# Kernel optimization log

Measured on AMD Instinct MI355X. Metric: run time of the kernel, lower is better.

Reference implementation:

```python
import jax, jax.numpy as jnp
import numpy as np

B = 1024      # graphs (frames)
P = 23        # nodes per frame (22 players + ball)
N = B * P     # total nodes
F = 14        # input node features
D = 256       # hidden dim
H = 4         # attention heads
Dh = D // H   # per-head dim
L = 3         # GATv2 layers
C = 23        # receiver classes
NEG_SLOPE = 0.2


def setup_inputs() -> dict:
    key = jax.random.key(0)
    ks = jax.random.split(key, 20)
    x = jax.random.normal(ks[0], (N, F), jnp.float32)
    # complete directed graph (no self loops) within each frame
    a = np.arange(P)
    s, d = np.meshgrid(a, a, indexing='ij')
    m = s != d
    s, d = s[m], d[m]                      # [P*(P-1)] = 506
    offs = (np.arange(B) * P)[:, None]
    src = (s[None, :] + offs).reshape(-1)
    dst = (d[None, :] + offs).reshape(-1)
    edge_index = jnp.asarray(np.stack([src, dst]), jnp.int32)   # [2, E]
    batch = jnp.asarray(np.repeat(np.arange(B), P), jnp.int32)  # [N]
    g = lambda k, shape, fan: jax.random.normal(k, shape, jnp.float32) / np.sqrt(fan)
    return {
        'x': x, 'edge_index': edge_index, 'batch': batch,
        # input projection F -> D
        'W_in': g(ks[1], (F, D), F), 'b_in': jnp.zeros((D,), jnp.float32),
        # stacked GATv2 layer params (all D -> D)
        'Wl': g(ks[2], (L, D, H, Dh), D), 'Wr': g(ks[3], (L, D, H, Dh), D),
        'att': g(ks[4], (L, H, Dh), Dh),
        # receiver head: D -> D -> C
        'Wr1': g(ks[5], (D, D), D), 'br1': jnp.zeros((D,), jnp.float32),
        'Wr2': g(ks[6], (D, C), D), 'br2': jnp.zeros((C,), jnp.float32),
        # shot head: receiver embedding + concat MLP 2D -> D -> 1
        'E_recv': g(ks[7], (C, D), D),
        'Ws1': g(ks[8], (2 * D, D), 2 * D), 'bs1': jnp.zeros((D,), jnp.float32),
        'Ws2': g(ks[9], (D, 1), D), 'bs2': jnp.zeros((1,), jnp.float32),
    }


def _gatv2_layer(h, src, dst, Wl, Wr, att):
    # GATv2: e_ij = a^T LeakyReLU(Wl h_j + Wr h_i); msg = alpha_ij * Wl h_j
    hl = jnp.einsum('nd,dhk->nhk', h, Wl)               # [N,H,Dh]
    hr = jnp.einsum('nd,dhk->nhk', h, Wr)
    e = jax.nn.leaky_relu(hl[src] + hr[dst], NEG_SLOPE) # [E,H,Dh]
    scores = jnp.einsum('ehk,hk->eh', e, att)           # [E,H]
    # segment softmax over incoming edges of each dst node
    smax = jax.ops.segment_max(scores, dst, num_segments=N)   # [N,H]
    ex = jnp.exp(scores - smax[dst])
    denom = jax.ops.segment_sum(ex, dst, num_segments=N)      # [N,H]
    alpha = ex / denom[dst]                                    # [E,H]
    msg = hl[src] * alpha[..., None]                           # [E,H,Dh]
    out = jax.ops.segment_sum(msg, dst, num_segments=N).reshape(N, H * Dh)
    return jax.nn.elu(out + h)  # residual + activation


def reference(x, edge_index, batch, W_in, b_in, Wl, Wr, att,
              Wr1, br1, Wr2, br2, E_recv, Ws1, bs1, Ws2, bs2):
    src, dst = edge_index[0], edge_index[1]
    h = x @ W_in + b_in                                   # [N,D]
    for l in range(L):
        h = _gatv2_layer(h, src, dst, Wl[l], Wr[l], att[l])
    # mean readout per graph
    cnt = jax.ops.segment_sum(jnp.ones((N,), h.dtype), batch, num_segments=B)
    g = jax.ops.segment_sum(h, batch, num_segments=B) / cnt[:, None]  # [B,D]
    # receiver distribution
    recv_logits = jax.nn.relu(g @ Wr1 + br1) @ Wr2 + br2  # [B,C]
    recv_probs = jax.nn.softmax(recv_logits, axis=1)
    # shot logit for every (graph, receiver) pair, fully batched
    z = jnp.concatenate([
        jnp.broadcast_to(g[:, None, :], (B, C, D)),
        jnp.broadcast_to(E_recv[None, :, :], (B, C, D)),
    ], axis=-1)                                           # [B,C,2D]
    shot_bc = (jax.nn.relu(z @ Ws1 + bs1) @ Ws2 + bs2)[..., 0]  # [B,C]
    # marginalize: expected shot logit under receiver distribution
    return jnp.sum(shot_bc * recv_probs, axis=1)          # [B]
```

## Files before the change

### kernel.cpp

```cpp
#include <hip/hip_runtime.h>

#define BBATCH 1024
#define NPAIR 512
#define PP 23
#define FF 14
#define DD 256
#define CC 23

#define HSTR 258
#define SLSTR 264
#define RG 47472
#define SL_OFF    (RG)
#define SRO_OFF   (RG + 12144)
#define FRAG_OFF  (RG)
#define ALPHA_OFF (RG + 24576)
#define XS_OFF    (ALPHA_OFF)
#define INVZ_OFF  (ALPHA_OFF + 8192)
#define SMEM_SZ   (INVZ_OFF + 384)

#define SWZB(b) ((b) ^ (((b) >> 3) & 7))
#define SWZC(c) (SWZB((c) >> 3) * 8 + ((c) & 7))

typedef _Float16 f16;
typedef __attribute__((ext_vector_type(8))) _Float16 f16x8;
typedef __attribute__((ext_vector_type(4))) _Float16 f16x4;
typedef __attribute__((ext_vector_type(2))) _Float16 f16x2;
typedef __attribute__((ext_vector_type(4))) float f32x4;

__global__ __launch_bounds__(256) void k_prep(const float* __restrict__ Wl,
    const float* __restrict__ Wr, const float* __restrict__ E,
    const float* __restrict__ Ws1, f16* __restrict__ Bf, float* __restrict__ EB)
{
    __shared__ float ws[DD][16];
    int t = threadIdx.x;
    if (blockIdx.x < 96) {
        int bid = blockIdx.x;
        int ll = bid >> 5, ntile = bid & 31;
        int n0 = ntile * 16;
        const float* W = (n0 < 256) ? (Wl + (size_t)ll * 65536) : (Wr + (size_t)ll * 65536);
        int c0 = n0 & 255;
        for (int kk = t >> 4; kk < DD; kk += 16)
            ws[kk][t & 15] = W[(size_t)kk * 256 + c0 + (t & 15)];
        __syncthreads();
        size_t base = (size_t)bid * 4096;
        for (int idx = t; idx < 4096; idx += 256) {
            int ks = idx >> 9;
            int lane = (idx >> 3) & 63;
            int e = idx & 7;
            int col = lane & 15;
            int k = ks * 32 + ((lane >> 4) << 3) + e;
            Bf[base + idx] = (f16)ws[k][col];
        }
    } else {
        int c = blockIdx.x - 96;
        float acc = 0.f;
        for (int k = 0; k < DD; ++k)
            acc = fmaf(E[c * DD + k], Ws1[(DD + k) * DD + t], acc);
        EB[c * DD + t] = acc;
    }
}

__global__ __launch_bounds__(512, 4) void k_fused(
    const float* __restrict__ x, const float* __restrict__ Win,
    const float* __restrict__ bin, const f16* __restrict__ Bf,
    const float* __restrict__ att, float* __restrict__ g)
{
    __shared__ __align__(16) char smem[SMEM_SZ];
    float* hstate = (float*)smem;
    f16* sl16   = (f16*)(smem + SL_OFF);
    f16* sro16  = (f16*)(smem + SRO_OFF);
    f16* frag   = (f16*)(smem + FRAG_OFF);
    f16* aF     = (f16*)(smem + ALPHA_OFF);
    float* xs   = (float*)(smem + XS_OFF);
    float* invZ = (float*)(smem + INVZ_OFF);

    int t = threadIdx.x;
    int pair = blockIdx.x;

    for (int idx = t; idx < 46 * FF; idx += 512)
        xs[idx] = x[(size_t)pair * 46 * FF + idx];
    __syncthreads();

    {
        int c2 = (t & 127) * 2, rp = t >> 7;
        float2 bb = *(const float2*)&bin[c2];
        for (int r = rp; r < 48; r += 4) {
            float h0 = 0.f, h1 = 0.f;
            if (r < 46) {
                h0 = bb.x; h1 = bb.y;
#pragma unroll
                for (int f = 0; f < FF; ++f) {
                    float xv = xs[r * FF + f];
                    float2 wv = *(const float2*)&Win[f * DD + c2];
                    h0 = fmaf(xv, wv.x, h0);
                    h1 = fmaf(xv, wv.y, h1);
                }
                *(float2*)&hstate[r * HSTR + c2] = make_float2(h0, h1);
            }
            int off = ((r >> 4) * 8 + (c2 >> 5)) * 512 +
                      ((r & 15) + (((c2 & 31) >> 3) << 4)) * 8 + (c2 & 7);
            f16x2 hv2 = { (f16)h0, (f16)h1 };
            *(f16x2*)(frag + off) = hv2;
        }
    }

    int ln = t & 63, w = t >> 6;

    int sc_i  = t >> 4;
    int sc_ch = t & 15;
    int sc_hh = sc_ch >> 2;
    bool sc_act = (t < 368);
    int sb0 = SWZB(2 * sc_ch) * 8;
    int sb1 = SWZB(2 * sc_ch + 1) * 8;

    for (int layer = 0; layer < 3; ++layer) {
        if (layer > 0) {
            int c2 = (t & 127) * 2, rp = t >> 7;
            for (int r = rp; r < 48; r += 4) {
                float h0 = 0.f, h1 = 0.f;
                if (r < 46) {
                    float2 hv = *(const float2*)&hstate[r * HSTR + c2];
                    h0 = hv.x; h1 = hv.y;
                }
                int off = ((r >> 4) * 8 + (c2 >> 5)) * 512 +
                          ((r & 15) + (((c2 & 31) >> 3) << 4)) * 8 + (c2 & 7);
                f16x2 hv2 = { (f16)h0, (f16)h1 };
                *(f16x2*)(frag + off) = hv2;
            }
        }
        __syncthreads();

        if (layer == 0)
            *(f32x4*)(smem + ALPHA_OFF + t * 16) = (f32x4)0.f;

        const f16* pB = Bf + (size_t)layer * 131072 + (size_t)(w * 4) * 4096 + ln * 8;
        const f16* lA = frag + ln * 8;

        f32x4 acc[3][4];
#pragma unroll
        for (int mt = 0; mt < 3; ++mt)
#pragma unroll
            for (int nt = 0; nt < 4; ++nt) acc[mt][nt] = (f32x4)0.0f;

        __builtin_amdgcn_s_setprio(1);
#pragma unroll
        for (int ks = 0; ks < 8; ++ks) {
            f16x8 a0 = *(const f16x8*)(lA + (0 * 8 + ks) * 512);
            f16x8 a1 = *(const f16x8*)(lA + (1 * 8 + ks) * 512);
            f16x8 a2 = *(const f16x8*)(lA + (2 * 8 + ks) * 512);
#pragma unroll
            for (int nt = 0; nt < 4; ++nt) {
                f16x8 b = *(const f16x8*)(pB + (nt * 8 + ks) * 512);
                acc[0][nt] = __builtin_amdgcn_mfma_f32_16x16x32_f16(a0, b, acc[0][nt], 0, 0, 0);
                acc[1][nt] = __builtin_amdgcn_mfma_f32_16x16x32_f16(a1, b, acc[1][nt], 0, 0, 0);
                acc[2][nt] = __builtin_amdgcn_mfma_f32_16x16x32_f16(a2, b, acc[2][nt], 0, 0, 0);
            }
        }
        __builtin_amdgcn_s_setprio(0);
        __syncthreads();

        for (int f = 0; f < 2; ++f) {
#pragma unroll
            for (int mt = 0; mt < 3; ++mt) {
                int rbase = mt * 16 + (ln >> 4) * 4;
#pragma unroll
                for (int nt = 0; nt < 4; ++nt) {
                    int col = w * 64 + nt * 16 + (ln & 15);
                    f16* dst = (col < 256) ? sl16 : sro16;
                    int cc = col & 255;
                    int sc = SWZC(cc);
#pragma unroll
                    for (int r2 = 0; r2 < 4; ++r2) {
                        int i = rbase + r2 - f * PP;
                        if (0 <= i && i < PP) dst[i * SLSTR + sc] = (f16)acc[mt][nt][r2];
                    }
                }
            }
            __syncthreads();

            if (sc_act) {
                const float* ap = att + layer * DD + sc_ch * 16;
                float4 af0 = *(const float4*)(ap);
                float4 af1 = *(const float4*)(ap + 4);
                float4 af2 = *(const float4*)(ap + 8);
                float4 af3 = *(const float4*)(ap + 12);
                f16x8 av0 = { (f16)af0.x, (f16)af0.y, (f16)af0.z, (f16)af0.w,
                              (f16)af1.x, (f16)af1.y, (f16)af1.z, (f16)af1.w };
                f16x8 av1 = { (f16)af2.x, (f16)af2.y, (f16)af2.z, (f16)af2.w,
                              (f16)af3.x, (f16)af3.y, (f16)af3.z, (f16)af3.w };
                const f16* srp = sro16 + sc_i * SLSTR;
                f16x8 rv0 = *(const f16x8*)(srp + sb0);
                f16x8 rv1 = *(const f16x8*)(srp + sb1);
                int wbase = ((sc_hh * 2 + (sc_i >> 4)) << 9) + ((sc_i & 15) << 3);
#pragma unroll 2
                for (int j = 0; j < PP; ++j) {
                    const f16* slp = sl16 + j * SLSTR;
                    f16x8 v0 = *(const f16x8*)(slp + sb0) + rv0;
                    f16x8 v1 = *(const f16x8*)(slp + sb1) + rv1;
                    v0 = __builtin_elementwise_max(v0, v0 * (f16)0.2f);
                    v1 = __builtin_elementwise_max(v1, v1 * (f16)0.2f);
                    f16x8 tot = av0 * v0;
                    tot += av1 * v1;
                    f16x4 t4 = __builtin_shufflevector(tot, tot, 0, 1, 2, 3) +
                               __builtin_shufflevector(tot, tot, 4, 5, 6, 7);
                    float p = (float)t4[0] + (float)t4[1] + (float)t4[2] + (float)t4[3];
                    p += __shfl_xor(p, 1, 64);
                    p += __shfl_xor(p, 2, 64);
                    if ((t & 3) == 0)
                        aF[wbase + ((j >> 3) << 7) + (j & 7)] =
                            (j == sc_i) ? (f16)(-60000.0f) : (f16)p;
                }
            }
            __syncthreads();

            if (t < 368) {
                int i = t >> 4, hh = (t >> 2) & 3, q = t & 3;
                int base = ((hh * 2 + (i >> 4)) << 9) + ((i & 15) << 3);
                float m = -1e30f;
                for (int j = q; j < PP; j += 4)
                    m = fmaxf(m, (float)aF[base + ((j >> 3) << 7) + (j & 7)]);
                m = fmaxf(m, __shfl_xor(m, 1, 64));
                m = fmaxf(m, __shfl_xor(m, 2, 64));
                float s = 0.f;
                for (int j = q; j < PP; j += 4) {
                    f16* p = aF + base + ((j >> 3) << 7) + (j & 7);
                    f16 e = (f16)__expf((float)*p - m);
                    *p = e;
                    s += (float)e;
                }
                s += __shfl_xor(s, 1, 64);
                s += __shfl_xor(s, 2, 64);
                if (q == 0) invZ[i * 4 + hh] = 1.f / s;
            }
            __syncthreads();

            {
                int h = w >> 1, mt = w & 1;
                f16x8 afrag = *(const f16x8*)(aF + ((h * 2 + mt) << 9) + ln * 8);
                int k0 = (ln >> 4) * 8;
                int cb = h * 64 + (ln & 15);
                __builtin_amdgcn_s_setprio(1);
#pragma unroll
                for (int nt = 0; nt < 4; ++nt) {
                    int c = cb + nt * 16;
                    int scn = SWZC(c);
                    f16x8 bfrag;
#pragma unroll
                    for (int e = 0; e < 8; ++e)
                        bfrag[e] = sl16[(k0 + e) * SLSTR + scn];
                    f32x4 a4 = __builtin_amdgcn_mfma_f32_16x16x32_f16(
                        afrag, bfrag, (f32x4)0.0f, 0, 0, 0);
#pragma unroll
                    for (int r2 = 0; r2 < 4; ++r2) {
                        int i = mt * 16 + (ln >> 4) * 4 + r2;
                        if (i < PP) {
                            int r = f * PP + i;
                            float res = a4[r2] * invZ[i * 4 + h] + hstate[r * HSTR + c];
                            hstate[r * HSTR + c] = (res > 0.f) ? res : (__expf(res) - 1.f);
                        }
                    }
                }
                __builtin_amdgcn_s_setprio(0);
            }
            __syncthreads();
        }
    }

    {
        int f = t >> 8, c = t & 255;
        float s = 0.f;
#pragma unroll
        for (int i = 0; i < PP; ++i) s += hstate[(f * PP + i) * HSTR + c];
        g[(size_t)(pair * 2 + f) * DD + c] = s * (1.0f / 23.0f);
    }
}

__global__ __launch_bounds__(256) void k_head(const float* __restrict__ g,
    const float* __restrict__ Wr1, const float* __restrict__ br1,
    const float* __restrict__ Wr2, const float* __restrict__ br2,
    const float* __restrict__ Ws1, const float* __restrict__ bs1,
    const float* __restrict__ Ws2, const float* __restrict__ bs2,
    const float* __restrict__ EB, float* __restrict__ out)
{
    __shared__ float gs[4][DD], t1s[4][DD], gtop[4][DD];
    __shared__ float logits[4][CC], probs[4][CC];
    __shared__ float red[4][4];
    int b0 = blockIdx.x * 4;
    int t = threadIdx.x;
    for (int idx = t; idx < 4 * DD; idx += 256)
        gs[idx >> 8][idx & 255] = g[(size_t)b0 * DD + idx];
    __syncthreads();

    float a1[4] = {0.f, 0.f, 0.f, 0.f}, a2[4] = {0.f, 0.f, 0.f, 0.f};
    for (int k = 0; k < DD; k += 2) {
        float w1a = Wr1[k * DD + t], w1b = Wr1[(k + 1) * DD + t];
        float w2a = Ws1[k * DD + t], w2b = Ws1[(k + 1) * DD + t];
#pragma unroll
        for (int gg = 0; gg < 4; ++gg) {
            float2 gv = *(const float2*)&gs[gg][k];
            a1[gg] = fmaf(gv.x, w1a, a1[gg]);
            a1[gg] = fmaf(gv.y, w1b, a1[gg]);
            a2[gg] = fmaf(gv.x, w2a, a2[gg]);
            a2[gg] = fmaf(gv.y, w2b, a2[gg]);
        }
    }
#pragma unroll
    for (int gg = 0; gg < 4; ++gg) {
        t1s[gg][t] = fmaxf(a1[gg] + br1[t], 0.f);
        gtop[gg][t] = a2[gg] + bs1[t];
    }
    __syncthreads();

    if (t < 4 * CC) {
        int gg = t / CC, c = t - gg * CC;
        float acc = br2[c];
        for (int d = 0; d < DD; ++d) acc = fmaf(t1s[gg][d], Wr2[d * CC + c], acc);
        logits[gg][c] = acc;
    }
    __syncthreads();
    if (t < 4 * CC) {
        int gg = t / CC, c = t - gg * CC;
        float m = -1e30f;
        for (int cc = 0; cc < CC; ++cc) m = fmaxf(m, logits[gg][cc]);
        float s = 0.f;
        for (int cc = 0; cc < CC; ++cc) s += __expf(logits[gg][cc] - m);
        probs[gg][c] = __expf(logits[gg][c] - m) / s;
    }
    __syncthreads();

    float wd = Ws2[t];
    float sacc[4];
#pragma unroll
    for (int gg = 0; gg < 4; ++gg) {
        float gt = gtop[gg][t];
        float acc = 0.f;
#pragma unroll
        for (int c = 0; c < CC; ++c)
            acc = fmaf(probs[gg][c], fmaxf(gt + EB[c * DD + t], 0.f), acc);
        sacc[gg] = acc * wd;
    }
#pragma unroll
    for (int gg = 0; gg < 4; ++gg) {
        float v = sacc[gg];
#pragma unroll
        for (int off = 32; off > 0; off >>= 1) v += __shfl_down(v, off, 64);
        if ((t & 63) == 0) red[t >> 6][gg] = v;
    }
    __syncthreads();
    if (t < 4)
        out[b0 + t] = red[0][t] + red[1][t] + red[2][t] + red[3][t] + bs2[0];
}

extern "C" void kernel_launch(void* const* d_in, const int* in_sizes, int n_in,
                              void* d_out, int out_size, void* d_ws, size_t ws_size,
                              hipStream_t stream)
{
    const float* x     = (const float*)d_in[0];
    const float* Win   = (const float*)d_in[3];
    const float* bin   = (const float*)d_in[4];
    const float* Wl    = (const float*)d_in[5];
    const float* Wr    = (const float*)d_in[6];
    const float* att   = (const float*)d_in[7];
    const float* Wr1   = (const float*)d_in[8];
    const float* br1   = (const float*)d_in[9];
    const float* Wr2   = (const float*)d_in[10];
    const float* br2   = (const float*)d_in[11];
    const float* Erecv = (const float*)d_in[12];
    const float* Ws1   = (const float*)d_in[13];
    const float* bs1   = (const float*)d_in[14];
    const float* Ws2   = (const float*)d_in[15];
    const float* bs2   = (const float*)d_in[16];
    float* out = (float*)d_out;

    f16* Bf   = (f16*)d_ws;
    float* g  = (float*)(Bf + (size_t)3 * 131072);
    float* EB = g + (size_t)BBATCH * DD;

    k_prep<<<dim3(96 + CC), dim3(256), 0, stream>>>(Wl, Wr, Erecv, Ws1, Bf, EB);
    k_fused<<<dim3(NPAIR), dim3(512), 0, stream>>>(x, Win, bin, Bf, att, g);
    k_head<<<dim3(256), dim3(256), 0, stream>>>(g, Wr1, br1, Wr2, br2,
                                                Ws1, bs1, Ws2, bs2, EB, out);
}
```

Before: 150.0 us.

## Fuse readout head MLPs into the main GATv2 kernel

Moves the receiver and shot head computation into the end of the fused GNN kernel, so each block computes its two graphs' outputs directly from the pooled embedding kept in shared memory. This removes the separate head kernel launch and the global round trip of the pooled features g. In exchange, each block now streams Wr1 and Ws1 itself for only two graphs instead of four, which raises total weight traffic through L2. It also reuses variables `ln` and `w`, which are presumably defined earlier in the kernel.

```diff
diff --git a/kernel.cpp b/kernel.cpp
--- a/kernel.cpp
+++ b/kernel.cpp
@@ -17,6 +17,13 @@
 #define XS_OFF    (ALPHA_OFF)
 #define INVZ_OFF  (ALPHA_OFF + 8192)
 #define SMEM_SZ   (INVZ_OFF + 384)
+
+#define GV_OFF    (ALPHA_OFF)
+#define T1_OFF    (ALPHA_OFF + 2048)
+#define GT_OFF    (ALPHA_OFF + 4096)
+#define LG_OFF    (ALPHA_OFF + 6144)
+#define PRB_OFF   (ALPHA_OFF + 6400)
+#define RED_OFF   (ALPHA_OFF + 6656)
 
 #define SWZB(b) ((b) ^ (((b) >> 3) & 7))
 #define SWZC(c) (SWZB((c) >> 3) * 8 + ((c) & 7))
@@ -63,7 +70,12 @@
 __global__ __launch_bounds__(512, 4) void k_fused(
     const float* __restrict__ x, const float* __restrict__ Win,
     const float* __restrict__ bin, const f16* __restrict__ Bf,
-    const float* __restrict__ att, float* __restrict__ g)
+    const float* __restrict__ att,
+    const float* __restrict__ Wr1, const float* __restrict__ br1,
+    const float* __restrict__ Wr2, const float* __restrict__ br2,
+    const float* __restrict__ Ws1, const float* __restrict__ bs1,
+    const float* __restrict__ Ws2, const float* __restrict__ bs2,
+    const float* __restrict__ EB, float* __restrict__ out)
 {
     __shared__ __align__(16) char smem[SMEM_SZ];
     float* hstate = (float*)smem;
@@ -73,6 +85,12 @@
     f16* aF     = (f16*)(smem + ALPHA_OFF);
     float* xs   = (float*)(smem + XS_OFF);
     float* invZ = (float*)(smem + INVZ_OFF);
+    float* gv   = (float*)(smem + GV_OFF);
+    float* t1s  = (float*)(smem + T1_OFF);
+    float* gts  = (float*)(smem + GT_OFF);
+    float* lgs  = (float*)(smem + LG_OFF);
+    float* prb  = (float*)(smem + PRB_OFF);
+    float* red  = (float*)(smem + RED_OFF);
 
     int t = threadIdx.x;
     int pair = blockIdx.x;
@@ -271,84 +289,63 @@
         float s = 0.f;
 #pragma unroll
         for (int i = 0; i < PP; ++i) s += hstate[(f * PP + i) * HSTR + c];
-        g[(size_t)(pair * 2 + f) * DD + c] = s * (1.0f / 23.0f);
-    }
-}
-
-__global__ __launch_bounds__(256) void k_head(const float* __restrict__ g,
-    const float* __restrict__ Wr1, const float* __restrict__ br1,
-    const float* __restrict__ Wr2, const float* __restrict__ br2,
-    const float* __restrict__ Ws1, const float* __restrict__ bs1,
-    const float* __restrict__ Ws2, const float* __restrict__ bs2,
-    const float* __restrict__ EB, float* __restrict__ out)
-{
-    __shared__ float gs[4][DD], t1s[4][DD], gtop[4][DD];
-    __shared__ float logits[4][CC], probs[4][CC];
-    __shared__ float red[4][4];
-    int b0 = blockIdx.x * 4;
-    int t = threadIdx.x;
-    for (int idx = t; idx < 4 * DD; idx += 256)
-        gs[idx >> 8][idx & 255] = g[(size_t)b0 * DD + idx];
-    __syncthreads();
-
-    float a1[4] = {0.f, 0.f, 0.f, 0.f}, a2[4] = {0.f, 0.f, 0.f, 0.f};
-    for (int k = 0; k < DD; k += 2) {
-        float w1a = Wr1[k * DD + t], w1b = Wr1[(k + 1) * DD + t];
-        float w2a = Ws1[k * DD + t], w2b = Ws1[(k + 1) * DD + t];
-#pragma unroll
-        for (int gg = 0; gg < 4; ++gg) {
-            float2 gv = *(const float2*)&gs[gg][k];
-            a1[gg] = fmaf(gv.x, w1a, a1[gg]);
-            a1[gg] = fmaf(gv.y, w1b, a1[gg]);
-            a2[gg] = fmaf(gv.x, w2a, a2[gg]);
-            a2[gg] = fmaf(gv.y, w2b, a2[gg]);
-        }
-    }
-#pragma unroll
-    for (int gg = 0; gg < 4; ++gg) {
-        t1s[gg][t] = fmaxf(a1[gg] + br1[t], 0.f);
-        gtop[gg][t] = a2[gg] + bs1[t];
-    }
-    __syncthreads();
-
-    if (t < 4 * CC) {
+        gv[f * 256 + c] = s * (1.0f / 23.0f);
+    }
+    __syncthreads();
+
+    {
+        int gg = t >> 8, c = t & 255;
+        const float* gp = gv + gg * 256;
+        float a1 = 0.f, a2 = 0.f;
+        for (int k = 0; k < DD; k += 2) {
+            float g0 = gp[k], g1 = gp[k + 1];
+            a1 = fmaf(g0, Wr1[k * DD + c], a1);
+            a1 = fmaf(g1, Wr1[(k + 1) * DD + c], a1);
+            a2 = fmaf(g0, Ws1[k * DD + c], a2);
+            a2 = fmaf(g1, Ws1[(k + 1) * DD + c], a2);
+        }
+        t1s[gg * 256 + c] = fmaxf(a1 + br1[c], 0.f);
+        gts[gg * 256 + c] = a2 + bs1[c];
+    }
+    __syncthreads();
+
+    if (t < 2 * CC) {
         int gg = t / CC, c = t - gg * CC;
         float acc = br2[c];
-        for (int d = 0; d < DD; ++d) acc = fmaf(t1s[gg][d], Wr2[d * CC + c], acc);
-        logits[gg][c] = acc;
-    }
-    __syncthreads();
-    if (t < 4 * CC) {
+        const float* tp = t1s + gg * 256;
+        for (int d = 0; d < DD; ++d) acc = fmaf(tp[d], Wr2[d * CC + c], acc);
+        lgs[gg * CC + c] = acc;
+    }
+    __syncthreads();
+
+    if (t < 2 * CC) {
         int gg = t / CC, c = t - gg * CC;
+        const float* lp = lgs + gg * CC;
         float m = -1e30f;
-        for (int cc = 0; cc < CC; ++cc) m = fmaxf(m, logits[gg][cc]);
+        for (int cc = 0; cc < CC; ++cc) m = fmaxf(m, lp[cc]);
         float s = 0.f;
-        for (int cc = 0; cc < CC; ++cc) s += __expf(logits[gg][cc] - m);
-        probs[gg][c] = __expf(logits[gg][c] - m) / s;
-    }
-    __syncthreads();
-
-    float wd = Ws2[t];
-    float sacc[4];
-#pragma unroll
-    for (int gg = 0; gg < 4; ++gg) {
-        float gt = gtop[gg][t];
+        for (int cc = 0; cc < CC; ++cc) s += __expf(lp[cc] - m);
+        prb[gg * CC + c] = __expf(lp[c] - m) / s;
+    }
+    __syncthreads();
+
+    {
+        int gg = t >> 8, c = t & 255;
+        float gt = gts[gg * 256 + c];
+        const float* pp = prb + gg * CC;
         float acc = 0.f;
 #pragma unroll
-        for (int c = 0; c < CC; ++c)
-            acc = fmaf(probs[gg][c], fmaxf(gt + EB[c * DD + t], 0.f), acc);
-        sacc[gg] = acc * wd;
-    }
-#pragma unroll
-    for (int gg = 0; gg < 4; ++gg) {
-        float v = sacc[gg];
-#pragma unroll
-        for (int off = 32; off > 0; off >>= 1) v += __shfl_down(v, off, 64);
-        if ((t & 63) == 0) red[t >> 6][gg] = v;
-    }
-    __syncthreads();
-    if (t < 4)
-        out[b0 + t] = red[0][t] + red[1][t] + red[2][t] + red[3][t] + bs2[0];
+        for (int cls = 0; cls < CC; ++cls)
+            acc = fmaf(pp[cls], fmaxf(gt + EB[cls * DD + c], 0.f), acc);
+        acc *= Ws2[c];
+#pragma unroll
+        for (int off = 32; off > 0; off >>= 1) acc += __shfl_down(acc, off, 64);
+        if (ln == 0) red[w] = acc;
+    }
+    __syncthreads();
+    if (t < 2)
+        out[pair * 2 + t] = red[t * 4] + red[t * 4 + 1] + red[t * 4 + 2] +
+                            red[t * 4 + 3] + bs2[0];
 }
 
 extern "C" void kernel_launch(void* const* d_in, const int* in_sizes, int n_in,
@@ -373,11 +370,9 @@
     float* out = (float*)d_out;
 
     f16* Bf   = (f16*)d_ws;
-    float* g  = (float*)(Bf + (size_t)3 * 131072);
-    float* EB = g + (size_t)BBATCH * DD;
+    float* EB = (float*)(Bf + (size_t)3 * 131072);
 
     k_prep<<<dim3(96 + CC), dim3(256), 0, stream>>>(Wl, Wr, Erecv, Ws1, Bf, EB);
-    k_fused<<<dim3(NPAIR), dim3(512), 0, stream>>>(x, Win, bin, Bf, att, g);
-    k_head<<<dim3(256), dim3(256), 0, stream>>>(g, Wr1, br1, Wr2, br2,
-                                                Ws1, bs1, Ws2, bs2, EB, out);
+    k_fused<<<dim3(NPAIR), dim3(512), 0, stream>>>(x, Win, bin, Bf, att,
+        Wr1, br1, Wr2, br2, Ws1, bs1, Ws2, bs2, EB, out);
 }
```

After: 145.7 us (median of 2 runs). -2.8%, faster.
